# Optimization experiments

Hardware: AMD Instinct MI355X
Metric: run time of the kernel (lower is better)

Reference implementation:

```python
import jax, jax.numpy as jnp
import numpy as np
import math

N_HEADS = 32
N_GROUPS = 8
D_HEAD = 64  # d_queries = d_values
D_MODEL = 2048


def _rope(x):
    # lucidrains-style interleaved RoPE over the full head dim, offset=0.
    # x: (B, H, S, D)
    S, D = x.shape[-2], x.shape[-1]
    inv_freq = 1.0 / (10000.0 ** (jnp.arange(0, D, 2, dtype=jnp.float32) / D))  # (D/2,)
    freqs = jnp.arange(S, dtype=jnp.float32)[:, None] * inv_freq[None, :]       # (S, D/2)
    cos = jnp.repeat(jnp.cos(freqs), 2, axis=-1)  # (S, D) interleaved
    sin = jnp.repeat(jnp.sin(freqs), 2, axis=-1)
    x2 = x.reshape(*x.shape[:-1], D // 2, 2)
    rot = jnp.stack([-x2[..., 1], x2[..., 0]], axis=-1).reshape(x.shape)
    return x * cos + rot * sin


def setup_inputs() -> dict:
    key = jax.random.key(0)
    ks = jax.random.split(key, 6)
    hidden_states = jax.random.normal(ks[0], (2, 2048, D_MODEL), dtype=jnp.float32)
    s = 0.02
    Wq = jax.random.normal(ks[1], (D_MODEL, N_HEADS * D_HEAD), dtype=jnp.float32) * s
    Wk = jax.random.normal(ks[2], (D_MODEL, N_GROUPS * D_HEAD), dtype=jnp.float32) * s
    Wv = jax.random.normal(ks[3], (D_MODEL, N_GROUPS * D_HEAD), dtype=jnp.float32) * s
    Wo = jax.random.normal(ks[4], (N_HEADS * D_HEAD, D_MODEL), dtype=jnp.float32) * s
    bo = jnp.zeros((D_MODEL,), dtype=jnp.float32)
    return {"hidden_states": hidden_states, "Wq": Wq, "Wk": Wk, "Wv": Wv, "Wo": Wo, "bo": bo}


def reference(hidden_states, Wq, Wk, Wv, Wo, bo):
    N, S, _ = hidden_states.shape
    n_rep = N_HEADS // N_GROUPS
    q = (hidden_states @ Wq).reshape(N, S, N_HEADS, D_HEAD).transpose(0, 2, 1, 3)
    k = (hidden_states @ Wk).reshape(N, S, N_GROUPS, D_HEAD).transpose(0, 2, 1, 3)
    v = (hidden_states @ Wv).reshape(N, S, N_GROUPS, D_HEAD).transpose(0, 2, 1, 3)
    q = _rope(q)
    k = _rope(k)
    # GQA: repeat_interleave KV heads
    k = jnp.repeat(k, n_rep, axis=1)
    v = jnp.repeat(v, n_rep, axis=1)
    scores = jnp.einsum('bhsd,bhtd->bhst', q, k)  # (B, H, S, S)
    # ALiBi bias added BEFORE scaling (matches source order)
    slopes = 2.0 ** (-(jnp.arange(1, N_HEADS + 1, dtype=jnp.float32) * 8.0 / N_HEADS))
    pos = jnp.arange(S, dtype=jnp.float32)
    alibi = -jnp.abs(pos[:, None] - pos[None, :])[None] * slopes[:, None, None]  # (H, S, S)
    scores = (scores + alibi[None]) / math.sqrt(D_HEAD)
    # grok-style rescaling
    scores = 30.0 * jnp.tanh(scores / 30.0)
    causal = jnp.tril(jnp.ones((S, S), dtype=bool))
    scores = jnp.where(causal[None, None], scores, -jnp.inf)
    probs = jax.nn.softmax(scores, axis=-1)
    ctx = jnp.einsum('bhst,bhtd->bhsd', probs, v)
    ctx = ctx.transpose(0, 2, 1, 3).reshape(N, S, N_HEADS * D_HEAD)
    return ctx @ Wo + bo
```

## Files before the change

kernel.cpp:

```cpp
#include <hip/hip_runtime.h>
#include <hip/hip_bf16.h>
#include <math.h>

#define DMODEL 2048
#define SEQ    2048
#define NH     32
#define NG     8
#define DH     64

typedef unsigned short u16;
typedef unsigned int u32;
using v8bf  = __attribute__((ext_vector_type(8))) __bf16;
using f32x4 = __attribute__((ext_vector_type(4))) float;

__device__ __forceinline__ float bf2f(u16 u) {
    unsigned int x = ((unsigned int)u) << 16;
    return __uint_as_float(x);
}
__device__ __forceinline__ u16 f2bf(float f) {
    unsigned int x = __float_as_uint(f);
    unsigned int r = (x + 0x7fffu + ((x >> 16) & 1u)) >> 16;
    return (u16)r;
}
__device__ __forceinline__ u16 f2bf_hw(float f) {
    __bf16 b = (__bf16)f;
    return __builtin_bit_cast(u16, b);
}
__device__ __forceinline__ u32 f2bf_pk(float lo, float hi) {
    return (u32)f2bf_hw(lo) | ((u32)f2bf_hw(hi) << 16);
}
__device__ __forceinline__ f32x4 mfma16(v8bf a, v8bf b, f32x4 c) {
    return __builtin_amdgcn_mfma_f32_16x16x32_bf16(a, b, c, 0, 0, 0);
}

#define LOG1E4_64 0.14391156509880297f
#define LOG2E     1.4426950408889634f

#define C_HS   0u
#define C_WQ   8388608u
#define C_WK   12582912u
#define C_WV   13631488u
#define C_WO   14680064u
#define C_BO   18874368u
#define W_Q    18876416u
#define W_K    27265024u
#define W_V    29362176u
#define W_CTX  31459328u

__device__ __forceinline__ bool detect_is_f32(const u16* hsu, int tid, float* red, int nw)
{
    ushort4 a = *(const ushort4*)(hsu + tid * 8);
    ushort4 b = *(const ushort4*)(hsu + tid * 8 + 4);
    u16 vals[8] = {a.x, a.y, a.z, a.w, b.x, b.y, b.z, b.w};
    float mymax = 0.0f;
    #pragma unroll
    for (int e = 0; e < 8; ++e) {
        float av = fabsf(bf2f(vals[e]));
        if (!(av < 1.0e30f)) av = 1.0e30f;
        mymax = fmaxf(mymax, av);
    }
    #pragma unroll
    for (int off = 1; off < 64; off <<= 1)
        mymax = fmaxf(mymax, __shfl_xor(mymax, off, 64));
    if ((tid & 63) == 0) red[tid >> 6] = mymax;
    __syncthreads();
    float m = red[0];
    for (int i = 1; i < nw; ++i) m = fmaxf(m, red[i]);
    __syncthreads();
    return m > 1.0e6f;
}

__global__ __launch_bounds__(256)
void conv_hs_bo(const void* __restrict__ hs, const void* __restrict__ bo,
                u16* __restrict__ canon)
{
    __shared__ float red[4];
    const int tid = threadIdx.x;
    const bool is_f32 = detect_is_f32((const u16*)hs, tid, red, 4);
    unsigned int g = (blockIdx.x * 256u + tid) * 8u;
    const void* src; unsigned int loc; u16* dst;
    if (g < 8388608u) { src = hs; loc = g;            dst = canon + C_HS + g; }
    else              { src = bo; loc = g - 8388608u; dst = canon + C_BO + loc; }

    ushort4 o0, o1;
    if (is_f32) {
        const float* f = (const float*)src + loc;
        float4 x = *(const float4*)f;
        float4 y = *(const float4*)(f + 4);
        o0.x = f2bf(x.x); o0.y = f2bf(x.y); o0.z = f2bf(x.z); o0.w = f2bf(x.w);
        o1.x = f2bf(y.x); o1.y = f2bf(y.y); o1.z = f2bf(y.z); o1.w = f2bf(y.w);
    } else {
        const u16* u = (const u16*)src + loc;
        o0 = *(const ushort4*)u;
        o1 = *(const ushort4*)(u + 4);
    }
    *(ushort4*)dst       = o0;
    *(ushort4*)(dst + 4) = o1;
}

__global__ __launch_bounds__(256)
void transp_w(const void* __restrict__ W, u16* __restrict__ dst,
              int K, int N, const u16* __restrict__ hs_orig)
{
    __shared__ float red[4];
    __shared__ u16 Ts[64][68];
    const int tid = threadIdx.x;
    const bool is_f32 = detect_is_f32(hs_orig, tid, red, 4);
    const int n0 = blockIdx.x * 64, k0 = blockIdx.y * 64;

    #pragma unroll
    for (int it = 0; it < 4; ++it) {
        int e  = tid + it * 256;
        int kr = e >> 4, n4 = (e & 15) << 2;
        if (is_f32) {
            const float* s = (const float*)W + (size_t)(k0 + kr) * N + n0 + n4;
            float4 x = *(const float4*)s;
            Ts[n4+0][kr] = f2bf(x.x); Ts[n4+1][kr] = f2bf(x.y);
            Ts[n4+2][kr] = f2bf(x.z); Ts[n4+3][kr] = f2bf(x.w);
        } else {
            ushort4 u = *(const ushort4*)((const u16*)W + (size_t)(k0 + kr) * N + n0 + n4);
            Ts[n4+0][kr] = u.x; Ts[n4+1][kr] = u.y;
            Ts[n4+2][kr] = u.z; Ts[n4+3][kr] = u.w;
        }
    }
    __syncthreads();
    #pragma unroll
    for (int it = 0; it < 4; ++it) {
        int e  = tid + it * 256;
        int nr = e >> 4, k4 = (e & 15) << 2;
        ushort4 u;
        u.x = Ts[nr][k4+0]; u.y = Ts[nr][k4+1];
        u.z = Ts[nr][k4+2]; u.w = Ts[nr][k4+3];
        *(ushort4*)(dst + (size_t)(n0 + nr) * K + k0 + k4) = u;
    }
}

__global__ __launch_bounds__(256)
void rope_table(float* __restrict__ c, float* __restrict__ s)
{
    int idx = blockIdx.x * 256 + threadIdx.x;
    int sq = idx >> 6, d = idx & 63;
    float freq = expf(-(float)(d & ~1) * LOG1E4_64);
    float sn, cs;
    sincosf((float)sq * freq, &sn, &cs);
    c[idx] = cs; s[idx] = sn;
}

__global__ __launch_bounds__(512, 4) __attribute__((amdgpu_waves_per_eu(4, 4)))
void gemm_qkv(const u16* __restrict__ hs, const u16* __restrict__ wqt,
              const u16* __restrict__ wkt, const u16* __restrict__ wvt,
              const float* __restrict__ ropec, const float* __restrict__ ropes,
              u16* __restrict__ qws, u16* __restrict__ kws, u16* __restrict__ vws)
{
    __shared__ __align__(16) u16 As[128][72];
    __shared__ __align__(16) u16 Bs[128][72];
    const int tid = threadIdx.x;
    const int w = tid >> 6, lane = tid & 63;
    const int l15 = lane & 15, quad = lane >> 4;
    const int wr = (w >> 2) * 64, wc = (w & 3) * 32;
    const int row0 = blockIdx.x * 128;
    const int n0   = blockIdx.y * 128;

    const u16* Wt; int nb, mode;
    if (n0 < 2048)      { Wt = wqt; nb = n0;        mode = 0; }
    else if (n0 < 2560) { Wt = wkt; nb = n0 - 2048; mode = 1; }
    else                { Wt = wvt; nb = n0 - 2560; mode = 2; }

    const int r0 = tid >> 3, c0 = (tid & 7) * 8;
    const u16* arow = hs + (size_t)(row0 + r0) * DMODEL + c0;
    const u16* brow = Wt + (size_t)(nb   + r0) * DMODEL + c0;

    f32x4 acc[4][2];
    #pragma unroll
    for (int mt = 0; mt < 4; ++mt)
        #pragma unroll
        for (int nt = 0; nt < 2; ++nt)
            acc[mt][nt] = (f32x4){0.f, 0.f, 0.f, 0.f};

    uint4 ra0, ra1, rb0, rb1;
#define LOADG(k0_) do {                                                       \
    ra0 = *(const uint4*)(arow + (k0_));                                      \
    ra1 = *(const uint4*)(arow + (size_t)64 * DMODEL + (k0_));                \
    rb0 = *(const uint4*)(brow + (k0_));                                      \
    rb1 = *(const uint4*)(brow + (size_t)64 * DMODEL + (k0_));                \
} while (0)
#define STORELDS() do {                                                       \
    *(uint4*)&As[r0][c0]      = ra0;                                          \
    *(uint4*)&As[r0 + 64][c0] = ra1;                                          \
    *(uint4*)&Bs[r0][c0]      = rb0;                                          \
    *(uint4*)&Bs[r0 + 64][c0] = rb1;                                          \
} while (0)

    LOADG(0);
    for (int k0 = 0; k0 < DMODEL; k0 += 64) {
        STORELDS();
        __syncthreads();
        if (k0 + 64 < DMODEL) LOADG(k0 + 64);
        #pragma unroll
        for (int ks = 0; ks < 2; ++ks) {
            v8bf a[4], b[2];
            #pragma unroll
            for (int mt = 0; mt < 4; ++mt)
                a[mt] = *(const v8bf*)&As[wr + 16*mt + l15][ks*32 + quad*8];
            #pragma unroll
            for (int nt = 0; nt < 2; ++nt)
                b[nt] = *(const v8bf*)&Bs[wc + 16*nt + l15][ks*32 + quad*8];
            #pragma unroll
            for (int mt = 0; mt < 4; ++mt)
                #pragma unroll
                for (int nt = 0; nt < 2; ++nt)
                    acc[mt][nt] = mfma16(a[mt], b[nt], acc[mt][nt]);
        }
        __syncthreads();
    }
#undef LOADG
#undef STORELDS

    #pragma unroll
    for (int mt = 0; mt < 4; ++mt) {
        #pragma unroll
        for (int nt = 0; nt < 2; ++nt) {
            int col  = n0 + wc + 16*nt + l15;
            int dcol = col & 63;
            #pragma unroll
            for (int reg = 0; reg < 4; ++reg) {
                int row = row0 + wr + 16*mt + quad*4 + reg;
                int b = row >> 11, s = row & (SEQ - 1);
                float val = acc[mt][nt][reg];
                if (mode < 2) {
                    float c2 = ropec[(s << 6) + dcol];
                    float s2 = ropes[(s << 6) + dcol];
                    float partner = __shfl_xor(val, 1, 64);
                    val = (dcol & 1) ? (val * c2 + partner * s2)
                                     : (val * c2 - partner * s2);
                }
                if (mode == 0) {
                    int h = col >> 6;
                    qws[((size_t)((b*NH + h) * SEQ + s)) * DH + dcol] = f2bf_hw(val);
                } else if (mode == 1) {
                    int g = (col - 2048) >> 6;
                    kws[((size_t)((b*NG + g) * SEQ + s)) * DH + dcol] = f2bf_hw(val);
                } else {
                    int g = (col - 2560) >> 6;
                    vws[((size_t)((b*NG + g) * DH + dcol)) * SEQ + s] = f2bf_hw(val);
                }
            }
        }
    }
}

__global__ __launch_bounds__(256, 4)
void attn(const u16* __restrict__ qws, const u16* __restrict__ kws,
          const u16* __restrict__ vws, u16* __restrict__ ctx)
{
    __shared__ __align__(16) u16 Ks[64][72];
    __shared__ __align__(16) u16 Vs[64][72];
    __shared__ __align__(16) u16 Ps[4][16][72];
    const int tid = threadIdx.x;
    const int w = tid >> 6, lane = tid & 63;
    const int l15 = lane & 15, quad = lane >> 4;
    const int sr = tid >> 3;
    const int sc = (tid & 7) * 8;

    const int h = blockIdx.y, b = blockIdx.z;
    const int g = h >> 2;

    const float slope = exp2f(-0.25f * (float)(h + 1));
    const u16* kbase  = kws + (size_t)(b*NG + g) * SEQ * DH;
    const u16* vtbase = vws + (size_t)(b*NG + g) * DH * SEQ;
    const u16* qhead  = qws + (size_t)(b*NH + h) * SEQ * DH;

    const float Ac = 0.125f * (LOG2E / 15.0f);
    const float Bc = -slope * 0.125f * (LOG2E / 15.0f);
    const float C3 = -60.0f * LOG2E;
    float bdw[4][4];
    #pragma unroll
    for (int mt = 0; mt < 4; ++mt)
        #pragma unroll
        for (int reg = 0; reg < 4; ++reg)
            bdw[mt][reg] = Bc * (float)((16*w + l15) - (16*mt + 4*quad + reg));

    uint4 rk0, rk1, rv0, rv1;

#define LOADG(kt_) do {                                                       \
    const u16* kp_ = kbase + (size_t)(kt_) * (64 * DH);                       \
    rk0 = *(const uint4*)(kp_ + sr * DH + sc);                                \
    rk1 = *(const uint4*)(kp_ + (sr + 32) * DH + sc);                         \
    const u16* vp_ = vtbase + (size_t)(kt_) * 64;                             \
    rv0 = *(const uint4*)(vp_ + (size_t)sr * SEQ + sc);                       \
    rv1 = *(const uint4*)(vp_ + (size_t)(sr + 32) * SEQ + sc);                \
} while (0)

#define STORELDS() do {                                                       \
    *(uint4*)&Ks[sr][sc]      = rk0;                                          \
    *(uint4*)&Ks[sr + 32][sc] = rk1;                                          \
    *(uint4*)&Vs[sr][sc]      = rv0;                                          \
    *(uint4*)&Vs[sr + 32][sc] = rv1;                                          \
} while (0)

#define COMPUTE(kt_, DIAGC) do {                                              \
    f32x4 sacc_[4];                                                           \
    _Pragma("unroll")                                                         \
    for (int mt_ = 0; mt_ < 4; ++mt_) sacc_[mt_] = (f32x4){0.f,0.f,0.f,0.f};  \
    _Pragma("unroll")                                                         \
    for (int ks_ = 0; ks_ < 2; ++ks_)                                         \
        _Pragma("unroll")                                                     \
        for (int mt_ = 0; mt_ < 4; ++mt_) {                                   \
            v8bf kf_ = *(const v8bf*)&Ks[16*mt_ + l15][ks_*32 + quad*8];      \
            sacc_[mt_] = mfma16(kf_, qa[ks_], sacc_[mt_]);                    \
        }                                                                     \
    const float tb_ = Bc * (float)(q0 - (kt_) * 64);                          \
    _Pragma("unroll")                                                         \
    for (int mt_ = 0; mt_ < 4; ++mt_) {                                       \
        float pv_[4];                                                         \
        _Pragma("unroll")                                                     \
        for (int rg_ = 0; rg_ < 4; ++rg_) {                                   \
            float arg_ = fmaf(sacc_[mt_][rg_], Ac, bdw[mt_][rg_] + tb_);      \
            float wv_  = __builtin_amdgcn_exp2f(arg_);                        \
            float rr_  = __builtin_amdgcn_rcpf(wv_ + 1.0f);                   \
            float p_   = __builtin_amdgcn_exp2f(rr_ * C3);                    \
            if (DIAGC && (16*mt_ + 4*quad + rg_) > (16*w + l15)) p_ = 0.0f;   \
            lsum += p_;                                                       \
            pv_[rg_] = p_;                                                    \
        }                                                                     \
        uint2 pk_;                                                            \
        pk_.x = f2bf_pk(pv_[0], pv_[1]);                                      \
        pk_.y = f2bf_pk(pv_[2], pv_[3]);                                      \
        *(uint2*)&Ps[w][l15][16*mt_ + quad*4] = pk_;                          \
    }                                                                         \
    _Pragma("unroll")                                                         \
    for (int ks_ = 0; ks_ < 2; ++ks_) {                                       \
        v8bf pa_ = *(const v8bf*)&Ps[w][l15][ks_*32 + quad*8];                \
        _Pragma("unroll")                                                     \
        for (int dt_ = 0; dt_ < 4; ++dt_) {                                   \
            v8bf vf_ = *(const v8bf*)&Vs[16*dt_ + l15][ks_*32 + quad*8];      \
            o[dt_] = mfma16(pa_, vf_, o[dt_]);                                \
        }                                                                     \
    }                                                                         \
} while (0)

    #pragma unroll 1
    for (int half = 0; half < 2; ++half) {
        const int qt = half ? 31 - (int)blockIdx.x : (int)blockIdx.x;
        const int q0 = qt * 64;

        const u16* qrow = qhead + (size_t)(q0 + 16*w + l15) * DH;
        v8bf qa[2];
        qa[0] = *(const v8bf*)(qrow + 0*32 + quad*8);
        qa[1] = *(const v8bf*)(qrow + 1*32 + quad*8);

        f32x4 o[4];
        #pragma unroll
        for (int dt = 0; dt < 4; ++dt) o[dt] = (f32x4){0.f, 0.f, 0.f, 0.f};
        float lsum = 0.0f;

        LOADG(0);
        for (int kt = 0; kt < qt; ++kt) {
            STORELDS();
            __syncthreads();
            LOADG(kt + 1);
            COMPUTE(kt, 0);
            __syncthreads();
        }
        STORELDS();
        __syncthreads();
        COMPUTE(qt, 1);
        __syncthreads();

        float lr = lsum;
        lr += __shfl_xor(lr, 16, 64);
        lr += __shfl_xor(lr, 32, 64);
        #pragma unroll
        for (int reg = 0; reg < 4; ++reg) {
            float linv = __builtin_amdgcn_rcpf(__shfl(lr, quad*4 + reg, 64));
            int s = q0 + 16*w + quad*4 + reg;
            u16* crow = ctx + (size_t)(b*SEQ + s) * DMODEL + h*64 + l15;
            #pragma unroll
            for (int dt = 0; dt < 4; ++dt)
                crow[16*dt] = f2bf_hw(o[dt][reg] * linv);
        }
    }
#undef LOADG
#undef STORELDS
#undef COMPUTE
}

__global__ __launch_bounds__(512, 4) __attribute__((amdgpu_waves_per_eu(4, 4)))
void oproj(const u16* __restrict__ ctx, const u16* __restrict__ wot,
           const u16* __restrict__ bo, const u16* __restrict__ hs_orig,
           void* __restrict__ outp)
{
    __shared__ float red[8];
    __shared__ __align__(16) u16 As[128][72];
    __shared__ __align__(16) u16 Bs[128][72];
    const int tid = threadIdx.x;
    const bool is_f32 = detect_is_f32(hs_orig, tid, red, 8);
    const int w = tid >> 6, lane = tid & 63;
    const int l15 = lane & 15, quad = lane >> 4;
    const int wr = (w >> 2) * 64, wc = (w & 3) * 32;
    const int row0 = blockIdx.x * 128;
    const int n0   = blockIdx.y * 128;

    const int r0 = tid >> 3, c0 = (tid & 7) * 8;
    const u16* arow = ctx + (size_t)(row0 + r0) * DMODEL + c0;
    const u16* brow = wot + (size_t)(n0   + r0) * DMODEL + c0;

    f32x4 acc[4][2];
    #pragma unroll
    for (int mt = 0; mt < 4; ++mt)
        #pragma unroll
        for (int nt = 0; nt < 2; ++nt)
            acc[mt][nt] = (f32x4){0.f, 0.f, 0.f, 0.f};

    uint4 ra0, ra1, rb0, rb1;
#define LOADG(k0_) do {                                                       \
    ra0 = *(const uint4*)(arow + (k0_));                                      \
    ra1 = *(const uint4*)(arow + (size_t)64 * DMODEL + (k0_));                \
    rb0 = *(const uint4*)(brow + (k0_));                                      \
    rb1 = *(const uint4*)(brow + (size_t)64 * DMODEL + (k0_));                \
} while (0)
#define STORELDS() do {                                                       \
    *(uint4*)&As[r0][c0]      = ra0;                                          \
    *(uint4*)&As[r0 + 64][c0] = ra1;                                          \
    *(uint4*)&Bs[r0][c0]      = rb0;                                          \
    *(uint4*)&Bs[r0 + 64][c0] = rb1;                                          \
} while (0)

    LOADG(0);
    for (int k0 = 0; k0 < DMODEL; k0 += 64) {
        STORELDS();
        __syncthreads();
        if (k0 + 64 < DMODEL) LOADG(k0 + 64);
        #pragma unroll
        for (int ks = 0; ks < 2; ++ks) {
            v8bf a[4], b[2];
            #pragma unroll
            for (int mt = 0; mt < 4; ++mt)
                a[mt] = *(const v8bf*)&As[wr + 16*mt + l15][ks*32 + quad*8];
            #pragma unroll
            for (int nt = 0; nt < 2; ++nt)
                b[nt] = *(const v8bf*)&Bs[wc + 16*nt + l15][ks*32 + quad*8];
            #pragma unroll
            for (int mt = 0; mt < 4; ++mt)
                #pragma unroll
                for (int nt = 0; nt < 2; ++nt)
                    acc[mt][nt] = mfma16(a[mt], b[nt], acc[mt][nt]);
        }
        __syncthreads();
    }
#undef LOADG
#undef STORELDS

    #pragma unroll
    for (int mt = 0; mt < 4; ++mt) {
        #pragma unroll
        for (int nt = 0; nt < 2; ++nt) {
            int col = n0 + wc + 16*nt + l15;
            float bias = bf2f(bo[col]);
            #pragma unroll
            for (int reg = 0; reg < 4; ++reg) {
                int row = row0 + wr + 16*mt + quad*4 + reg;
                float val = acc[mt][nt][reg] + bias;
                if (is_f32) ((float*)outp)[(size_t)row * DMODEL + col] = val;
                else        ((u16*)outp)[(size_t)row * DMODEL + col]   = f2bf(val);
            }
        }
    }
}

extern "C" void kernel_launch(void* const* d_in, const int* in_sizes, int n_in,
                              void* d_out, int out_size, void* d_ws, size_t ws_size,
                              hipStream_t stream) {
    u16* ws = (u16*)d_ws;
    u16* canon = ws;
    u16* qws = ws + W_Q;
    u16* kws = ws + W_K;
    u16* vws = ws + W_V;
    u16* ctxp = ws + W_CTX;
    float* ropec = (float*)(ws + W_CTX);
    float* ropes = ropec + SEQ * DH;
    const u16* hs_raw = (const u16*)d_in[0];

    conv_hs_bo<<<dim3(4097), 256, 0, stream>>>(d_in[0], d_in[5], canon);
    transp_w<<<dim3(32, 32), 256, 0, stream>>>(d_in[1], canon + C_WQ, 2048, 2048, hs_raw);
    transp_w<<<dim3(8, 32),  256, 0, stream>>>(d_in[2], canon + C_WK, 2048, 512, hs_raw);
    transp_w<<<dim3(8, 32),  256, 0, stream>>>(d_in[3], canon + C_WV, 2048, 512, hs_raw);
    transp_w<<<dim3(32, 32), 256, 0, stream>>>(d_in[4], canon + C_WO, 2048, 2048, hs_raw);
    rope_table<<<dim3(512), 256, 0, stream>>>(ropec, ropes);
    gemm_qkv<<<dim3(32, 24), 512, 0, stream>>>(canon + C_HS, canon + C_WQ,
        canon + C_WK, canon + C_WV, ropec, ropes, qws, kws, vws);
    attn<<<dim3(16, NH, 2), 256, 0, stream>>>(qws, kws, vws, ctxp);
    oproj<<<dim3(32, 16), 512, 0, stream>>>(ctxp, canon + C_WO, canon + C_BO, hs_raw, d_out);
}
```

Baseline: 339.9 us.

## Use direct global-to-LDS loads in GEMMs and merge prep kernels into one launch

Both projection GEMMs now stage A/B tiles through global_load_lds (buffer-to-LDS DMA) instead of loading into registers and storing to LDS. The padded 72-wide LDS rows become unpadded 64-wide rows. The register-level prefetch of the next tile is removed, so the global load is no longer overlapped with MFMA compute. The four weight transposes and the RoPE table build are folded into a single launch with a z-dimension to cut launch overhead. Risks are LDS bank conflicts from the unpadded layout and exposed load latency without double buffering.

```diff
diff --git a/kernel.cpp b/kernel.cpp
--- a/kernel.cpp
+++ b/kernel.cpp
@@ -31,6 +31,11 @@
 }
 __device__ __forceinline__ f32x4 mfma16(v8bf a, v8bf b, f32x4 c) {
     return __builtin_amdgcn_mfma_f32_16x16x32_bf16(a, b, c, 0, 0, 0);
+}
+__device__ __forceinline__ void gload16(const u16* g, u16* l) {
+    __builtin_amdgcn_global_load_lds(
+        (const __attribute__((address_space(1))) void*)g,
+        (__attribute__((address_space(3))) void*)l, 16, 0, 0);
 }
 
 #define LOG1E4_64 0.14391156509880297f
@@ -99,14 +104,38 @@
 }
 
 __global__ __launch_bounds__(256)
-void transp_w(const void* __restrict__ W, u16* __restrict__ dst,
-              int K, int N, const u16* __restrict__ hs_orig)
+void transp_all(const void* __restrict__ Wq, const void* __restrict__ Wk,
+                const void* __restrict__ Wv, const void* __restrict__ Wo,
+                u16* __restrict__ canon, const u16* __restrict__ hs_orig,
+                float* __restrict__ ropec, float* __restrict__ ropes)
 {
     __shared__ float red[4];
     __shared__ u16 Ts[64][68];
     const int tid = threadIdx.x;
+    const int z = blockIdx.z;
+
+    if (z == 4) {
+        int bid = blockIdx.y * 32 + blockIdx.x;
+        if (bid >= 512) return;
+        int idx = bid * 256 + tid;
+        int sq = idx >> 6, d = idx & 63;
+        float freq = expf(-(float)(d & ~1) * LOG1E4_64);
+        float sn, cs;
+        sincosf((float)sq * freq, &sn, &cs);
+        ropec[idx] = cs; ropes[idx] = sn;
+        return;
+    }
+
+    const void* W; u16* dst; int N;
+    if (z == 0)      { W = Wq; dst = canon + C_WQ; N = 2048; }
+    else if (z == 1) { W = Wk; dst = canon + C_WK; N = 512;  }
+    else if (z == 2) { W = Wv; dst = canon + C_WV; N = 512;  }
+    else             { W = Wo; dst = canon + C_WO; N = 2048; }
+    const int n0 = blockIdx.x * 64, k0 = blockIdx.y * 64;
+    if (n0 >= N) return;
+    const int K = 2048;
+
     const bool is_f32 = detect_is_f32(hs_orig, tid, red, 4);
-    const int n0 = blockIdx.x * 64, k0 = blockIdx.y * 64;
 
     #pragma unroll
     for (int it = 0; it < 4; ++it) {
@@ -135,25 +164,14 @@
     }
 }
 
-__global__ __launch_bounds__(256)
-void rope_table(float* __restrict__ c, float* __restrict__ s)
-{
-    int idx = blockIdx.x * 256 + threadIdx.x;
-    int sq = idx >> 6, d = idx & 63;
-    float freq = expf(-(float)(d & ~1) * LOG1E4_64);
-    float sn, cs;
-    sincosf((float)sq * freq, &sn, &cs);
-    c[idx] = cs; s[idx] = sn;
-}
-
 __global__ __launch_bounds__(512, 4) __attribute__((amdgpu_waves_per_eu(4, 4)))
 void gemm_qkv(const u16* __restrict__ hs, const u16* __restrict__ wqt,
               const u16* __restrict__ wkt, const u16* __restrict__ wvt,
               const float* __restrict__ ropec, const float* __restrict__ ropes,
               u16* __restrict__ qws, u16* __restrict__ kws, u16* __restrict__ vws)
 {
-    __shared__ __align__(16) u16 As[128][72];
-    __shared__ __align__(16) u16 Bs[128][72];
+    __shared__ __align__(16) u16 As[128 * 64];
+    __shared__ __align__(16) u16 Bs[128 * 64];
     const int tid = threadIdx.x;
     const int w = tid >> 6, lane = tid & 63;
     const int l15 = lane & 15, quad = lane >> 4;
@@ -166,9 +184,15 @@
     else if (n0 < 2560) { Wt = wkt; nb = n0 - 2048; mode = 1; }
     else                { Wt = wvt; nb = n0 - 2560; mode = 2; }
 
-    const int r0 = tid >> 3, c0 = (tid & 7) * 8;
-    const u16* arow = hs + (size_t)(row0 + r0) * DMODEL + c0;
-    const u16* brow = Wt + (size_t)(nb   + r0) * DMODEL + c0;
+    const int crow = lane >> 3, ccol = (lane & 7) * 8;
+    const u16* ga0 = hs + (size_t)(row0 + 16*w +     crow) * DMODEL + ccol;
+    const u16* ga1 = hs + (size_t)(row0 + 16*w + 8 + crow) * DMODEL + ccol;
+    const u16* gb0 = Wt + (size_t)(nb   + 16*w +     crow) * DMODEL + ccol;
+    const u16* gb1 = Wt + (size_t)(nb   + 16*w + 8 + crow) * DMODEL + ccol;
+    u16* la0 = &As[(16*w    ) * 64];
+    u16* la1 = &As[(16*w + 8) * 64];
+    u16* lb0 = &Bs[(16*w    ) * 64];
+    u16* lb1 = &Bs[(16*w + 8) * 64];
 
     f32x4 acc[4][2];
     #pragma unroll
@@ -177,34 +201,21 @@
         for (int nt = 0; nt < 2; ++nt)
             acc[mt][nt] = (f32x4){0.f, 0.f, 0.f, 0.f};
 
-    uint4 ra0, ra1, rb0, rb1;
-#define LOADG(k0_) do {                                                       \
-    ra0 = *(const uint4*)(arow + (k0_));                                      \
-    ra1 = *(const uint4*)(arow + (size_t)64 * DMODEL + (k0_));                \
-    rb0 = *(const uint4*)(brow + (k0_));                                      \
-    rb1 = *(const uint4*)(brow + (size_t)64 * DMODEL + (k0_));                \
-} while (0)
-#define STORELDS() do {                                                       \
-    *(uint4*)&As[r0][c0]      = ra0;                                          \
-    *(uint4*)&As[r0 + 64][c0] = ra1;                                          \
-    *(uint4*)&Bs[r0][c0]      = rb0;                                          \
-    *(uint4*)&Bs[r0 + 64][c0] = rb1;                                          \
-} while (0)
-
-    LOADG(0);
     for (int k0 = 0; k0 < DMODEL; k0 += 64) {
-        STORELDS();
-        __syncthreads();
-        if (k0 + 64 < DMODEL) LOADG(k0 + 64);
+        gload16(ga0 + k0, la0);
+        gload16(ga1 + k0, la1);
+        gload16(gb0 + k0, lb0);
+        gload16(gb1 + k0, lb1);
+        __syncthreads();
         #pragma unroll
         for (int ks = 0; ks < 2; ++ks) {
             v8bf a[4], b[2];
             #pragma unroll
             for (int mt = 0; mt < 4; ++mt)
-                a[mt] = *(const v8bf*)&As[wr + 16*mt + l15][ks*32 + quad*8];
+                a[mt] = *(const v8bf*)&As[(wr + 16*mt + l15) * 64 + ks*32 + quad*8];
             #pragma unroll
             for (int nt = 0; nt < 2; ++nt)
-                b[nt] = *(const v8bf*)&Bs[wc + 16*nt + l15][ks*32 + quad*8];
+                b[nt] = *(const v8bf*)&Bs[(wc + 16*nt + l15) * 64 + ks*32 + quad*8];
             #pragma unroll
             for (int mt = 0; mt < 4; ++mt)
                 #pragma unroll
@@ -213,8 +224,6 @@
         }
         __syncthreads();
     }
-#undef LOADG
-#undef STORELDS
 
     #pragma unroll
     for (int mt = 0; mt < 4; ++mt) {
@@ -391,8 +400,8 @@
            void* __restrict__ outp)
 {
     __shared__ float red[8];
-    __shared__ __align__(16) u16 As[128][72];
-    __shared__ __align__(16) u16 Bs[128][72];
+    __shared__ __align__(16) u16 As[128 * 64];
+    __shared__ __align__(16) u16 Bs[128 * 64];
     const int tid = threadIdx.x;
     const bool is_f32 = detect_is_f32(hs_orig, tid, red, 8);
     const int w = tid >> 6, lane = tid & 63;
@@ -401,9 +410,15 @@
     const int row0 = blockIdx.x * 128;
     const int n0   = blockIdx.y * 128;
 
-    const int r0 = tid >> 3, c0 = (tid & 7) * 8;
-    const u16* arow = ctx + (size_t)(row0 + r0) * DMODEL + c0;
-    const u16* brow = wot + (size_t)(n0   + r0) * DMODEL + c0;
+    const int crow = lane >> 3, ccol = (lane & 7) * 8;
+    const u16* ga0 = ctx + (size_t)(row0 + 16*w +     crow) * DMODEL + ccol;
+    const u16* ga1 = ctx + (size_t)(row0 + 16*w + 8 + crow) * DMODEL + ccol;
+    const u16* gb0 = wot + (size_t)(n0   + 16*w +     crow) * DMODEL + ccol;
+    const u16* gb1 = wot + (size_t)(n0   + 16*w + 8 + crow) * DMODEL + ccol;
+    u16* la0 = &As[(16*w    ) * 64];
+    u16* la1 = &As[(16*w + 8) * 64];
+    u16* lb0 = &Bs[(16*w    ) * 64];
+    u16* lb1 = &Bs[(16*w + 8) * 64];
 
     f32x4 acc[4][2];
     #pragma unroll
@@ -412,34 +427,21 @@
         for (int nt = 0; nt < 2; ++nt)
             acc[mt][nt] = (f32x4){0.f, 0.f, 0.f, 0.f};
 
-    uint4 ra0, ra1, rb0, rb1;
-#define LOADG(k0_) do {                                                       \
-    ra0 = *(const uint4*)(arow + (k0_));                                      \
-    ra1 = *(const uint4*)(arow + (size_t)64 * DMODEL + (k0_));                \
-    rb0 = *(const uint4*)(brow + (k0_));                                      \
-    rb1 = *(const uint4*)(brow + (size_t)64 * DMODEL + (k0_));                \
-} while (0)
-#define STORELDS() do {                                                       \
-    *(uint4*)&As[r0][c0]      = ra0;                                          \
-    *(uint4*)&As[r0 + 64][c0] = ra1;                                          \
-    *(uint4*)&Bs[r0][c0]      = rb0;                                          \
-    *(uint4*)&Bs[r0 + 64][c0] = rb1;                                          \
-} while (0)
-
-    LOADG(0);
     for (int k0 = 0; k0 < DMODEL; k0 += 64) {
-        STORELDS();
-        __syncthreads();
-        if (k0 + 64 < DMODEL) LOADG(k0 + 64);
+        gload16(ga0 + k0, la0);
+        gload16(ga1 + k0, la1);
+        gload16(gb0 + k0, lb0);
+        gload16(gb1 + k0, lb1);
+        __syncthreads();
         #pragma unroll
         for (int ks = 0; ks < 2; ++ks) {
             v8bf a[4], b[2];
             #pragma unroll
             for (int mt = 0; mt < 4; ++mt)
-                a[mt] = *(const v8bf*)&As[wr + 16*mt + l15][ks*32 + quad*8];
+                a[mt] = *(const v8bf*)&As[(wr + 16*mt + l15) * 64 + ks*32 + quad*8];
             #pragma unroll
             for (int nt = 0; nt < 2; ++nt)
-                b[nt] = *(const v8bf*)&Bs[wc + 16*nt + l15][ks*32 + quad*8];
+                b[nt] = *(const v8bf*)&Bs[(wc + 16*nt + l15) * 64 + ks*32 + quad*8];
             #pragma unroll
             for (int mt = 0; mt < 4; ++mt)
                 #pragma unroll
@@ -448,8 +450,6 @@
         }
         __syncthreads();
     }
-#undef LOADG
-#undef STORELDS
 
     #pragma unroll
     for (int mt = 0; mt < 4; ++mt) {
@@ -482,11 +482,8 @@
     const u16* hs_raw = (const u16*)d_in[0];
 
     conv_hs_bo<<<dim3(4097), 256, 0, stream>>>(d_in[0], d_in[5], canon);
-    transp_w<<<dim3(32, 32), 256, 0, stream>>>(d_in[1], canon + C_WQ, 2048, 2048, hs_raw);
-    transp_w<<<dim3(8, 32),  256, 0, stream>>>(d_in[2], canon + C_WK, 2048, 512, hs_raw);
-    transp_w<<<dim3(8, 32),  256, 0, stream>>>(d_in[3], canon + C_WV, 2048, 512, hs_raw);
-    transp_w<<<dim3(32, 32), 256, 0, stream>>>(d_in[4], canon + C_WO, 2048, 2048, hs_raw);
-    rope_table<<<dim3(512), 256, 0, stream>>>(ropec, ropes);
+    transp_all<<<dim3(32, 32, 5), 256, 0, stream>>>(d_in[1], d_in[2], d_in[3],
+        d_in[4], canon, hs_raw, ropec, ropes);
     gemm_qkv<<<dim3(32, 24), 512, 0, stream>>>(canon + C_HS, canon + C_WQ,
         canon + C_WK, canon + C_WV, ropec, ropes, qws, kws, vws);
     attn<<<dim3(16, NH, 2), 256, 0, stream>>>(qws, kws, vws, ctxp);
```

After: 361.1 us. 6.2% more time.
